# Performance work log

Measured on AMD Instinct MI355X. Metric: run time of the kernel, lower is better.

The kernel has to match this reference:

```python
import jax, jax.numpy as jnp
import numpy as np

N = 10000      # nodes
E = 160000     # edges
C = 72         # hidden dim = 18 * mul (mul=4)
A = 16         # node_attr dim (16x0e)
L = 3          # layers
O = 64         # output dim (64x0e)
B = 16         # graphs in batch
IN_DIM = 18    # irreps_node_input dim
SH = 9         # spherical harmonics dim, lmax=2
FC = 100       # radial MLP hidden (fc_neurons=[1,100])
MAX_RADIUS = 2.0
NUM_NEIGHBORS = 16.0
NUM_NODES = 625.0


def sph_harm_l2(d):
    # component-normalized real spherical harmonics up to l=2 on unit vectors d [E,3]
    x, y, z = d[:, 0], d[:, 1], d[:, 2]
    s3, s5, s15 = 3.0 ** 0.5, 5.0 ** 0.5, 15.0 ** 0.5
    return jnp.stack([
        jnp.ones_like(x),
        s3 * x, s3 * y, s3 * z,
        s15 * x * y, s15 * y * z, (s5 / 2.0) * (3.0 * z * z - 1.0),
        s15 * x * z, (s15 / 2.0) * (x * x - y * y),
    ], axis=1)  # [E, 9]


def setup_inputs() -> dict:
    key = jax.random.key(0)
    ks = jax.random.split(key, 16)
    pos = jax.random.normal(ks[0], (N, 3), dtype=jnp.float32)
    node_attr = jax.random.normal(ks[1], (N, A), dtype=jnp.float32)
    batch = jnp.sort(jax.random.randint(ks[2], (N,), 0, B))
    edge_src = jax.random.randint(ks[3], (E,), 0, N)
    edge_dst = jax.random.randint(ks[4], (E,), 0, N)
    W_in = jax.random.normal(ks[5], (IN_DIM, C), dtype=jnp.float32) / np.sqrt(IN_DIM)
    W_tp = jax.random.normal(ks[6], (L, SH, C, C), dtype=jnp.float32) / np.sqrt(C)
    W_self = jax.random.normal(ks[7], (L, C, C), dtype=jnp.float32) / np.sqrt(C)
    W_attr = jax.random.normal(ks[8], (L, A, C), dtype=jnp.float32) / np.sqrt(A)
    fc1_w = jax.random.normal(ks[9], (L, 1, FC), dtype=jnp.float32)
    fc1_b = jnp.zeros((L, FC), dtype=jnp.float32)
    fc2_w = jax.random.normal(ks[10], (L, FC, SH), dtype=jnp.float32) / np.sqrt(FC)
    W_out = jax.random.normal(ks[11], (C, O), dtype=jnp.float32) / np.sqrt(C)
    return {"pos": pos, "node_attr": node_attr, "batch": batch,
            "edge_src": edge_src, "edge_dst": edge_dst,
            "W_in": W_in, "W_tp": W_tp, "W_self": W_self, "W_attr": W_attr,
            "fc1_w": fc1_w, "fc1_b": fc1_b, "fc2_w": fc2_w, "W_out": W_out}


def reference(pos, node_attr, batch, edge_src, edge_dst,
              W_in, W_tp, W_self, W_attr, fc1_w, fc1_b, fc2_w, W_out):
    n = pos.shape[0]
    # edge geometry
    rvec = pos[edge_src] - pos[edge_dst]                      # [E,3]
    r = jnp.linalg.norm(rvec, axis=1, keepdims=True)          # [E,1]
    dvec = rvec / jnp.maximum(r, 1e-9)
    sh = sph_harm_l2(dvec)                                    # [E,9]
    # single cosine radial basis with cutoff at max_radius (number_of_basis=1)
    t = r / MAX_RADIUS
    emb = jnp.where(t < 1.0, jnp.cos(0.5 * jnp.pi * t), 0.0)  # [E,1]
    # node inputs: fixed one-hot on the scalar channel, embedded to hidden dim
    onehot = jnp.zeros((IN_DIM,), dtype=pos.dtype).at[0].set(1.0)
    h = jnp.broadcast_to((onehot @ W_in)[None, :], (n, C))    # [N,C]
    for l in range(L):
        # radial MLP -> per-edge, per-SH-path weights
        u = jax.nn.silu(emb @ fc1_w[l] + fc1_b[l]) @ fc2_w[l]  # [E,9]
        path = u * sh                                          # [E,9]
        hs = h[edge_src]                                       # [E,C]
        m = jnp.zeros_like(hs)
        for s in range(SH):  # fixed small set of tensor-product paths
            m = m + path[:, s:s + 1] * (hs @ W_tp[l, s])       # [E,C]
        agg = jax.ops.segment_sum(m, edge_dst, num_segments=n) / np.sqrt(NUM_NEIGHBORS)
        h = jax.nn.gelu(agg + h @ W_self[l] + node_attr @ W_attr[l])
    out_nodes = h @ W_out                                      # [N,O]
    pooled = jax.ops.segment_sum(out_nodes, batch, num_segments=B)
    return pooled / np.sqrt(NUM_NODES)                         # [B,O]
```

## Files before the change

kernel.cpp:

```cpp
#include <hip/hip_runtime.h>
#include <math.h>

#define NN 10000
#define NE 160000
#define CC 72
#define AA 16
#define LL 3
#define OO 64
#define NBATCH 16
#define SH 9
#define FCN 100
#define KK (SH*CC)
#define KA 736
#define KP 768
#define KG 96
#define NT 5
#define PSU 16
#define NB 1024

typedef __attribute__((ext_vector_type(8))) short bf16x8;
typedef __attribute__((ext_vector_type(4))) float f32x4;

static __device__ __forceinline__ float gelu_tanh(float x) {
    float x3 = x * x * x;
    float inner = 0.7978845608028654f * (x + 0.044715f * x3);
    return 0.5f * x * (1.0f + tanhf(inner));
}
static __device__ __forceinline__ unsigned short f2bf(float x) {
    unsigned int u = __float_as_uint(x);
    u += 0x7FFFu + ((u >> 16) & 1u);
    return (unsigned short)(u >> 16);
}
static __device__ __forceinline__ float bf2f(unsigned short u) {
    return __uint_as_float((unsigned int)u << 16);
}
static __device__ __forceinline__ unsigned int pack2bf(float lo, float hi) {
    return (unsigned int)f2bf(lo) | ((unsigned int)f2bf(hi) << 16);
}
static __device__ __forceinline__ float bfLo(unsigned int u) {
    return __uint_as_float(u << 16);
}
static __device__ __forceinline__ float bfHi(unsigned int u) {
    return __uint_as_float(u & 0xffff0000u);
}

__global__ void k_zero(int* __restrict__ cnt) {
    int i = blockIdx.x * blockDim.x + threadIdx.x;
    if (i < NN) cnt[i] = 0;
}

#define GB_HIST 625
#define GB_UTAB 13
#define GB_WCAT 180
#define GB_INIT 704
#define GB_PREP (GB_HIST + GB_UTAB + GB_WCAT + GB_INIT)

__global__ __launch_bounds__(256) void k_prep(
        const float* __restrict__ pos, const int* __restrict__ esrc,
        const int* __restrict__ edst, int* __restrict__ cnt,
        const float* __restrict__ fc1w, const float* __restrict__ fc1b,
        const float* __restrict__ fc2w, float* __restrict__ U,
        const float* __restrict__ Wtp, const float* __restrict__ Wself,
        const float* __restrict__ Wattr, unsigned short* __restrict__ Wb,
        const float* __restrict__ W_in, unsigned short* __restrict__ h0) {
    int bb = blockIdx.x, t = threadIdx.x;
    if (bb < GB_HIST) {
        int e = bb * 256 + t;
        if (e < NE) {
            int s = esrc[e], d = edst[e];
            float dx = pos[3 * s] - pos[3 * d];
            float dy = pos[3 * s + 1] - pos[3 * d + 1];
            float dz = pos[3 * s + 2] - pos[3 * d + 2];
            float r = sqrtf(dx * dx + dy * dy + dz * dz);
            if (r * 0.5f < 1.0f) atomicAdd(&cnt[d], 1);
        }
        return;
    }
    bb -= GB_HIST;
    if (bb < GB_UTAB) {
        int i = bb * 256 + t;
        if (i < LL * (NB + 1)) {
            int l = i / (NB + 1), b = i - l * (NB + 1);
            float emb = cosf(1.5707963267948966f * ((float)b / (float)NB));
            float u[SH];
#pragma unroll
            for (int q = 0; q < SH; ++q) u[q] = 0.f;
            const float* w1 = &fc1w[l * FCN];
            const float* b1 = &fc1b[l * FCN];
            const float* w2 = &fc2w[l * FCN * SH];
            for (int f = 0; f < FCN; ++f) {
                float a = emb * w1[f] + b1[f];
                float si = a / (1.0f + expf(-a));
#pragma unroll
                for (int q = 0; q < SH; ++q) u[q] += si * w2[f * SH + q];
            }
            float* ud = &U[(size_t)i * 12];
#pragma unroll
            for (int q = 0; q < SH; ++q) ud[q] = u[q];
            ud[9] = 0.f; ud[10] = 0.f; ud[11] = 0.f;
        }
        return;
    }
    bb -= GB_UTAB;
    if (bb < GB_WCAT) {
        int i0 = (bb * 256 + t) * 4;
#pragma unroll
        for (int u = 0; u < 4; ++u) {
            int i = i0 + u;
            int l = i / (NT * KG * 128);
            int rem = i - l * (NT * KG * 128);
            int nt = rem / (KG * 128); rem -= nt * (KG * 128);
            int kg = rem / 128; int e = rem - kg * 128;
            int n = nt * 16 + (e >> 3);
            int k = kg * 8 + (e & 7);
            float v = 0.f;
            if (n < CC && k < KA) {
                if (k < KK)            v = 0.25f * Wtp[(size_t)l * KK * CC + k * CC + n];
                else if (k < KK + CC)  v = Wself[(size_t)l * CC * CC + (k - KK) * CC + n];
                else                   v = Wattr[(size_t)l * AA * CC + (k - KK - CC) * CC + n];
            }
            Wb[i] = f2bf(v);
        }
        return;
    }
    bb -= GB_WCAT;
    {
        int i0 = (bb * 256 + t) * 4;
#pragma unroll
        for (int u = 0; u < 4; ++u) {
            int i = i0 + u;
            if (i < NN * CC) h0[i] = f2bf(W_in[i % CC]);
        }
    }
}

__global__ void k_scan(const int* __restrict__ cnt, int* __restrict__ off,
                       int* __restrict__ cur, float* __restrict__ hp) {
    __shared__ int sa[256], sb[256];
    const int PER = 40;
    int t = threadIdx.x;
    int base = t * PER;
    int loc[PER];
    int run = 0;
#pragma unroll
    for (int i = 0; i < PER; ++i) {
        int idx = base + i;
        int v = (idx < NN) ? cnt[idx] : 0;
        loc[i] = run;
        run += v;
    }
    sa[t] = run;
    __syncthreads();
    int* in = sa; int* out = sb;
    for (int o = 1; o < 256; o <<= 1) {
        int v = in[t];
        if (t >= o) v += in[t - o];
        out[t] = v;
        __syncthreads();
        int* tmp = in; in = out; out = tmp;
    }
    int ebase = (t > 0) ? in[t - 1] : 0;
#pragma unroll
    for (int i = 0; i < PER; ++i) {
        int idx = base + i;
        if (idx <= NN) {
            int v = ebase + loc[i];
            off[idx] = v;
            if (idx < NN) cur[idx] = v;
        }
    }
    for (int i = t; i < NBATCH * CC; i += 256) hp[i] = 0.f;
}

__global__ __launch_bounds__(256) void k_scatter3(const float* __restrict__ pos,
                                                  const int* __restrict__ esrc,
                                                  const int* __restrict__ edst,
                                                  int* __restrict__ cur,
                                                  int* __restrict__ src_s,
                                                  const float* __restrict__ U,
                                                  unsigned short* __restrict__ path) {
    int e = blockIdx.x * blockDim.x + threadIdx.x;
    if (e >= NE) return;
    int s = esrc[e], d = edst[e];
    float dx = pos[3 * s] - pos[3 * d];
    float dy = pos[3 * s + 1] - pos[3 * d + 1];
    float dz = pos[3 * s + 2] - pos[3 * d + 2];
    float r = sqrtf(dx * dx + dy * dy + dz * dz);
    if (r * 0.5f >= 1.0f) return;
    int slot = atomicAdd(&cur[d], 1);
    src_s[slot] = s;

    float inv = 1.0f / fmaxf(r, 1e-9f);
    float x = dx * inv, y = dy * inv, z = dz * inv;
    const float s3 = 1.7320508075688772f;
    const float s5 = 2.23606797749979f;
    const float s15 = 3.872983346207417f;
    float sh[SH];
    sh[0] = 1.0f;
    sh[1] = s3 * x;
    sh[2] = s3 * y;
    sh[3] = s3 * z;
    sh[4] = s15 * x * y;
    sh[5] = s15 * y * z;
    sh[6] = 0.5f * s5 * (3.0f * z * z - 1.0f);
    sh[7] = s15 * x * z;
    sh[8] = 0.5f * s15 * (x * x - y * y);

    float fb = r * 0.5f * (float)NB;
    int b0 = (int)fb;
    float fr = fb - (float)b0;

#pragma unroll
    for (int l = 0; l < LL; ++l) {
        const float* t0 = &U[((size_t)l * (NB + 1) + b0) * 12];
        float4 a0 = *(const float4*)(t0 + 0);
        float4 a1 = *(const float4*)(t0 + 4);
        float  a2 = t0[8];
        float4 c0 = *(const float4*)(t0 + 12);
        float4 c1 = *(const float4*)(t0 + 16);
        float  c2 = t0[20];
        float u0 = (a0.x + fr * (c0.x - a0.x)) * sh[0];
        float u1 = (a0.y + fr * (c0.y - a0.y)) * sh[1];
        float u2 = (a0.z + fr * (c0.z - a0.z)) * sh[2];
        float u3 = (a0.w + fr * (c0.w - a0.w)) * sh[3];
        float u4 = (a1.x + fr * (c1.x - a1.x)) * sh[4];
        float u5 = (a1.y + fr * (c1.y - a1.y)) * sh[5];
        float u6 = (a1.z + fr * (c1.z - a1.z)) * sh[6];
        float u7 = (a1.w + fr * (c1.w - a1.w)) * sh[7];
        float u8 = (a2   + fr * (c2   - a2))   * sh[8];
        unsigned short* pd = &path[((size_t)l * NE + slot) * PSU];
        uint4 w0, w1;
        w0.x = pack2bf(u0, u1); w0.y = pack2bf(u2, u3);
        w0.z = pack2bf(u4, u5); w0.w = pack2bf(u6, u7);
        w1.x = pack2bf(u8, 0.f); w1.y = 0u; w1.z = 0u; w1.w = 0u;
        *(uint4*)pd = w0;
        *(uint4*)(pd + 8) = w1;
    }
}

__global__ __launch_bounds__(1024, 8) void k_layer(
        const unsigned short* __restrict__ h,
        const float* __restrict__ attr,
        const unsigned short* __restrict__ path_l,
        const int* __restrict__ src_s,
        const int* __restrict__ off,
        const unsigned short* __restrict__ Wb,
        unsigned short* __restrict__ hout) {
    __shared__ unsigned short Alds[KG * 128];
    int t = threadIdx.x, w = t >> 6, lane = t & 63;
    int n0 = blockIdx.x * 16;
    int d = n0 + w;
    int db = off[d], de = off[d + 1];

    bool act = lane < 36;
    int c2 = 2 * lane;
    float a1[SH], a2[SH];
#pragma unroll
    for (int q = 0; q < SH; ++q) { a1[q] = 0.f; a2[q] = 0.f; }

    for (int i = db; i < de; i += 4) {
        int m = de - i;
        unsigned int hv[4];
        uint4 pa[4];
        unsigned int pb[4];
#pragma unroll
        for (int j = 0; j < 4; ++j) {
            if (j < m) {
                int s = src_s[i + j];
                pa[j] = *(const uint4*)&path_l[(size_t)(i + j) * PSU];
                pb[j] = *(const unsigned int*)&path_l[(size_t)(i + j) * PSU + 8];
                if (act) hv[j] = *(const unsigned int*)&h[(size_t)s * CC + c2];
            }
        }
#pragma unroll
        for (int j = 0; j < 4; ++j) {
            if (j < m) {
                float lo = act ? bfLo(hv[j]) : 0.f;
                float hi = act ? bfHi(hv[j]) : 0.f;
                float p0 = bfLo(pa[j].x), p1 = bfHi(pa[j].x);
                float p2 = bfLo(pa[j].y), p3 = bfHi(pa[j].y);
                float p4 = bfLo(pa[j].z), p5 = bfHi(pa[j].z);
                float p6 = bfLo(pa[j].w), p7 = bfHi(pa[j].w);
                float p8 = bfLo(pb[j]);
                a1[0] += p0 * lo; a2[0] += p0 * hi;
                a1[1] += p1 * lo; a2[1] += p1 * hi;
                a1[2] += p2 * lo; a2[2] += p2 * hi;
                a1[3] += p3 * lo; a2[3] += p3 * hi;
                a1[4] += p4 * lo; a2[4] += p4 * hi;
                a1[5] += p5 * lo; a2[5] += p5 * hi;
                a1[6] += p6 * lo; a2[6] += p6 * hi;
                a1[7] += p7 * lo; a2[7] += p7 * hi;
                a1[8] += p8 * lo; a2[8] += p8 * hi;
            }
        }
    }

    if (act) {
        int kgo = lane >> 2, kjo = 2 * (lane & 3);
        int hb = w * 8 + kjo;
#pragma unroll
        for (int q = 0; q < SH; ++q)
            *(unsigned int*)&Alds[(9 * q + kgo) * 128 + hb] = pack2bf(a1[q], a2[q]);
        *(unsigned int*)&Alds[(81 + kgo) * 128 + hb] =
            *(const unsigned int*)&h[(size_t)d * CC + c2];
        if (lane < 8)
            *(unsigned int*)&Alds[(90 + kgo) * 128 + hb] =
                pack2bf(attr[(size_t)d * AA + c2], attr[(size_t)d * AA + c2 + 1]);
    }
    if (lane < 16)
        *(unsigned int*)&Alds[(92 + (lane >> 2)) * 128 + w * 8 + 2 * (lane & 3)] = 0u;
    __syncthreads();

    if (w < NT) {
        const unsigned short* Ab = Alds + (lane & 15) * 8;
        const unsigned short* Bb = Wb + ((size_t)w * KG) * 128 + (lane & 15) * 8;
        f32x4 acc = (f32x4){0.f, 0.f, 0.f, 0.f};
#pragma unroll
        for (int s = 0; s < 24; ++s) {
            int kg = s * 4 + (lane >> 4);
            bf16x8 af = *(const bf16x8*)(Ab + (size_t)kg * 128);
            bf16x8 bq = *(const bf16x8*)(Bb + (size_t)kg * 128);
            acc = __builtin_amdgcn_mfma_f32_16x16x32_bf16(af, bq, acc, 0, 0, 0);
        }
        int cb = lane & 15, rb = (lane >> 4) * 4;
        int row = n0 + rb, col = w * 16 + cb;
        if (col < CC) {
#pragma unroll
            for (int j = 0; j < 4; ++j)
                hout[(size_t)(row + j) * CC + col] = f2bf(gelu_tanh(acc[j]));
        }
    }
}

__global__ __launch_bounds__(256) void k_pool(const unsigned short* __restrict__ h,
                                              const int* __restrict__ batch,
                                              float* __restrict__ hp) {
    __shared__ float sp[NBATCH * CC];
    int t = threadIdx.x;
    for (int i = t; i < NBATCH * CC; i += 256) sp[i] = 0.f;
    __syncthreads();
    int n0 = blockIdx.x * 16;
    for (int i = t; i < 16 * CC; i += 256) {
        int nl = i / CC, c = i - nl * CC;
        int n = n0 + nl;
        if (n < NN) atomicAdd(&sp[batch[n] * CC + c], bf2f(h[(size_t)n * CC + c]));
    }
    __syncthreads();
    for (int i = t; i < NBATCH * CC; i += 256) {
        float v = sp[i];
        if (v != 0.f) atomicAdd(&hp[i], v);
    }
}

__global__ __launch_bounds__(1024) void k_outmm(const float* __restrict__ hp,
                                                const float* __restrict__ Wout,
                                                float* __restrict__ out) {
    __shared__ float hs[NBATCH * CC];
    int t = threadIdx.x;
    for (int i = t; i < NBATCH * CC; i += 1024) hs[i] = hp[i];
    __syncthreads();
    int b = t >> 6, o = t & 63;
    float acc = 0.f;
#pragma unroll 8
    for (int c = 0; c < CC; ++c) acc += hs[b * CC + c] * Wout[c * OO + o];
    out[t] = acc * (1.0f / 25.0f);
}

extern "C" void kernel_launch(void* const* d_in, const int* in_sizes, int n_in,
                              void* d_out, int out_size, void* d_ws, size_t ws_size,
                              hipStream_t stream) {
    const float* pos       = (const float*)d_in[0];
    const float* node_attr = (const float*)d_in[1];
    const int*   batch     = (const int*)d_in[2];
    const int*   esrc      = (const int*)d_in[3];
    const int*   edst      = (const int*)d_in[4];
    const float* W_in      = (const float*)d_in[5];
    const float* W_tp      = (const float*)d_in[6];
    const float* W_self    = (const float*)d_in[7];
    const float* W_attr    = (const float*)d_in[8];
    const float* fc1w      = (const float*)d_in[9];
    const float* fc1b      = (const float*)d_in[10];
    const float* fc2w      = (const float*)d_in[11];
    const float* W_out     = (const float*)d_in[12];
    float* out = (float*)d_out;

    char* p = (char*)d_ws;
    auto alloc = [&](size_t bytes) -> void* {
        void* r = (void*)p;
        p += (bytes + 255) & ~(size_t)255;
        return r;
    };
    int*   cnt   = (int*)alloc((size_t)NN * 4);
    int*   cur   = (int*)alloc((size_t)NN * 4);
    float* hp    = (float*)alloc((size_t)NBATCH * CC * 4);
    int*   off   = (int*)alloc((size_t)(NN + 1) * 4);
    int*   src_s = (int*)alloc((size_t)NE * 4);
    unsigned short* path = (unsigned short*)alloc((size_t)LL * NE * PSU * 2);
    float* U     = (float*)alloc((size_t)LL * (NB + 1) * 12 * 4);
    unsigned short* Wb = (unsigned short*)alloc((size_t)LL * NT * KG * 128 * 2);
    unsigned short* h0 = (unsigned short*)alloc((size_t)NN * CC * 2);
    unsigned short* h1 = (unsigned short*)alloc((size_t)NN * CC * 2);

    k_zero<<<(NN + 255) / 256, 256, 0, stream>>>(cnt);
    k_prep<<<GB_PREP, 256, 0, stream>>>(pos, esrc, edst, cnt, fc1w, fc1b, fc2w, U,
                                        W_tp, W_self, W_attr, Wb, W_in, h0);
    k_scan<<<1, 256, 0, stream>>>(cnt, off, cur, hp);
    k_scatter3<<<(NE + 255) / 256, 256, 0, stream>>>(pos, esrc, edst, cur, src_s, U, path);

    const unsigned short* hin = h0;
    unsigned short* hout = h1;
    for (int l = 0; l < LL; ++l) {
        k_layer<<<NN / 16, 1024, 0, stream>>>(hin, node_attr,
                                              path + (size_t)l * NE * PSU, src_s, off,
                                              Wb + (size_t)l * NT * KG * 128, hout);
        const unsigned short* tmp = hin; hin = hout; hout = (unsigned short*)tmp;
    }
    k_pool<<<(NN + 15) / 16, 256, 0, stream>>>(hin, batch, hp);
    k_outmm<<<1, 1024, 0, stream>>>(hp, W_out, out);
}
```

Before: 161.2 us.

## Stage block's per-edge path weights in LDS and deepen gather unroll to 8

Each block now copies the contiguous path-weight rows for all edges of its 16 destination nodes into shared memory in chunks, using cooperative vector loads. Each wave then reads the path weights from LDS instead of issuing redundant per-lane global loads. The gather of source features is unrolled to 8 edges for more memory-level parallelism. In exchange it adds block-wide barriers per chunk, extra LDS usage, and possible load imbalance across waves within a chunk.

```diff
diff --git a/kernel.cpp b/kernel.cpp
--- a/kernel.cpp
+++ b/kernel.cpp
@@ -17,6 +17,7 @@
 #define NT 5
 #define PSU 16
 #define NB 1024
+#define EMAX 176
 
 typedef __attribute__((ext_vector_type(8))) short bf16x8;
 typedef __attribute__((ext_vector_type(4))) float f32x4;
@@ -246,10 +247,12 @@
         const int* __restrict__ off,
         const unsigned short* __restrict__ Wb,
         unsigned short* __restrict__ hout) {
+    __shared__ unsigned short Plds[EMAX * PSU];
     __shared__ unsigned short Alds[KG * 128];
     int t = threadIdx.x, w = t >> 6, lane = t & 63;
     int n0 = blockIdx.x * 16;
     int d = n0 + w;
+    int b0 = off[n0], e0 = off[n0 + 16];
     int db = off[d], de = off[d + 1];
 
     bool act = lane < 36;
@@ -258,41 +261,51 @@
 #pragma unroll
     for (int q = 0; q < SH; ++q) { a1[q] = 0.f; a2[q] = 0.f; }
 
-    for (int i = db; i < de; i += 4) {
-        int m = de - i;
-        unsigned int hv[4];
-        uint4 pa[4];
-        unsigned int pb[4];
-#pragma unroll
-        for (int j = 0; j < 4; ++j) {
-            if (j < m) {
-                int s = src_s[i + j];
-                pa[j] = *(const uint4*)&path_l[(size_t)(i + j) * PSU];
-                pb[j] = *(const unsigned int*)&path_l[(size_t)(i + j) * PSU + 8];
-                if (act) hv[j] = *(const unsigned int*)&h[(size_t)s * CC + c2];
+    for (int base = b0; base < e0; base += EMAX) {
+        int nE = min(EMAX, e0 - base);
+        const uint4* p4 = (const uint4*)(path_l + (size_t)base * PSU);
+        uint4* Pl4 = (uint4*)Plds;
+        for (int idx = t; idx < nE * 2; idx += 1024)
+            Pl4[idx] = p4[idx];
+        __syncthreads();
+        int lb = db > base ? db : base;
+        int le = de < base + nE ? de : base + nE;
+        for (int i = lb; i < le; i += 8) {
+            int m = le - i;
+            unsigned int hv[8];
+#pragma unroll
+            for (int j = 0; j < 8; ++j) {
+                if (j < m && act) {
+                    int s = src_s[i + j];
+                    hv[j] = *(const unsigned int*)&h[(size_t)s * CC + c2];
+                }
             }
-        }
-#pragma unroll
-        for (int j = 0; j < 4; ++j) {
-            if (j < m) {
-                float lo = act ? bfLo(hv[j]) : 0.f;
-                float hi = act ? bfHi(hv[j]) : 0.f;
-                float p0 = bfLo(pa[j].x), p1 = bfHi(pa[j].x);
-                float p2 = bfLo(pa[j].y), p3 = bfHi(pa[j].y);
-                float p4 = bfLo(pa[j].z), p5 = bfHi(pa[j].z);
-                float p6 = bfLo(pa[j].w), p7 = bfHi(pa[j].w);
-                float p8 = bfLo(pb[j]);
-                a1[0] += p0 * lo; a2[0] += p0 * hi;
-                a1[1] += p1 * lo; a2[1] += p1 * hi;
-                a1[2] += p2 * lo; a2[2] += p2 * hi;
-                a1[3] += p3 * lo; a2[3] += p3 * hi;
-                a1[4] += p4 * lo; a2[4] += p4 * hi;
-                a1[5] += p5 * lo; a2[5] += p5 * hi;
-                a1[6] += p6 * lo; a2[6] += p6 * hi;
-                a1[7] += p7 * lo; a2[7] += p7 * hi;
-                a1[8] += p8 * lo; a2[8] += p8 * hi;
+#pragma unroll
+            for (int j = 0; j < 8; ++j) {
+                if (j < m) {
+                    const unsigned short* p = &Plds[(i + j - base) * PSU];
+                    uint4 pw = *(const uint4*)p;
+                    unsigned int pz = *(const unsigned int*)(p + 8);
+                    float lo = act ? bfLo(hv[j]) : 0.f;
+                    float hi = act ? bfHi(hv[j]) : 0.f;
+                    float p0 = bfLo(pw.x), p1 = bfHi(pw.x);
+                    float p2 = bfLo(pw.y), p3 = bfHi(pw.y);
+                    float p4v = bfLo(pw.z), p5 = bfHi(pw.z);
+                    float p6 = bfLo(pw.w), p7 = bfHi(pw.w);
+                    float p8 = bfLo(pz);
+                    a1[0] += p0 * lo;  a2[0] += p0 * hi;
+                    a1[1] += p1 * lo;  a2[1] += p1 * hi;
+                    a1[2] += p2 * lo;  a2[2] += p2 * hi;
+                    a1[3] += p3 * lo;  a2[3] += p3 * hi;
+                    a1[4] += p4v * lo; a2[4] += p4v * hi;
+                    a1[5] += p5 * lo;  a2[5] += p5 * hi;
+                    a1[6] += p6 * lo;  a2[6] += p6 * hi;
+                    a1[7] += p7 * lo;  a2[7] += p7 * hi;
+                    a1[8] += p8 * lo;  a2[8] += p8 * hi;
+                }
             }
         }
+        __syncthreads();
     }
 
     if (act) {
```

Result: faster. 138.5 us (-14.1%).

## Store compact per-edge geometry and recompute path weights inside layer kernel

Applied to the files above, without the earlier changes.

The scatter kernel now writes one 16-byte record per edge (source index, bf16 direction, radial bin position) instead of a source index array plus three layers of 32-byte bf16 path-weight rows. Each layer kernel rebuilds the spherical harmonics and interpolates the radial lookup table itself. This shrinks scatter writes and per-layer edge reads, at the cost of extra ALU work and table loads in the layer loop. The unit-direction components are now rounded to bf16, which changes precision slightly.

```diff
diff --git a/kernel.cpp b/kernel.cpp
--- a/kernel.cpp
+++ b/kernel.cpp
@@ -12,10 +12,8 @@
 #define FCN 100
 #define KK (SH*CC)
 #define KA 736
-#define KP 768
 #define KG 96
 #define NT 5
-#define PSU 16
 #define NB 1024
 
 typedef __attribute__((ext_vector_type(8))) short bf16x8;
@@ -172,13 +170,11 @@
     for (int i = t; i < NBATCH * CC; i += 256) hp[i] = 0.f;
 }
 
-__global__ __launch_bounds__(256) void k_scatter3(const float* __restrict__ pos,
+__global__ __launch_bounds__(256) void k_scatter4(const float* __restrict__ pos,
                                                   const int* __restrict__ esrc,
                                                   const int* __restrict__ edst,
                                                   int* __restrict__ cur,
-                                                  int* __restrict__ src_s,
-                                                  const float* __restrict__ U,
-                                                  unsigned short* __restrict__ path) {
+                                                  uint4* __restrict__ geom) {
     int e = blockIdx.x * blockDim.x + threadIdx.x;
     if (e >= NE) return;
     int s = esrc[e], d = edst[e];
@@ -188,62 +184,23 @@
     float r = sqrtf(dx * dx + dy * dy + dz * dz);
     if (r * 0.5f >= 1.0f) return;
     int slot = atomicAdd(&cur[d], 1);
-    src_s[slot] = s;
-
     float inv = 1.0f / fmaxf(r, 1e-9f);
     float x = dx * inv, y = dy * inv, z = dz * inv;
-    const float s3 = 1.7320508075688772f;
-    const float s5 = 2.23606797749979f;
-    const float s15 = 3.872983346207417f;
-    float sh[SH];
-    sh[0] = 1.0f;
-    sh[1] = s3 * x;
-    sh[2] = s3 * y;
-    sh[3] = s3 * z;
-    sh[4] = s15 * x * y;
-    sh[5] = s15 * y * z;
-    sh[6] = 0.5f * s5 * (3.0f * z * z - 1.0f);
-    sh[7] = s15 * x * z;
-    sh[8] = 0.5f * s15 * (x * x - y * y);
-
     float fb = r * 0.5f * (float)NB;
-    int b0 = (int)fb;
-    float fr = fb - (float)b0;
-
-#pragma unroll
-    for (int l = 0; l < LL; ++l) {
-        const float* t0 = &U[((size_t)l * (NB + 1) + b0) * 12];
-        float4 a0 = *(const float4*)(t0 + 0);
-        float4 a1 = *(const float4*)(t0 + 4);
-        float  a2 = t0[8];
-        float4 c0 = *(const float4*)(t0 + 12);
-        float4 c1 = *(const float4*)(t0 + 16);
-        float  c2 = t0[20];
-        float u0 = (a0.x + fr * (c0.x - a0.x)) * sh[0];
-        float u1 = (a0.y + fr * (c0.y - a0.y)) * sh[1];
-        float u2 = (a0.z + fr * (c0.z - a0.z)) * sh[2];
-        float u3 = (a0.w + fr * (c0.w - a0.w)) * sh[3];
-        float u4 = (a1.x + fr * (c1.x - a1.x)) * sh[4];
-        float u5 = (a1.y + fr * (c1.y - a1.y)) * sh[5];
-        float u6 = (a1.z + fr * (c1.z - a1.z)) * sh[6];
-        float u7 = (a1.w + fr * (c1.w - a1.w)) * sh[7];
-        float u8 = (a2   + fr * (c2   - a2))   * sh[8];
-        unsigned short* pd = &path[((size_t)l * NE + slot) * PSU];
-        uint4 w0, w1;
-        w0.x = pack2bf(u0, u1); w0.y = pack2bf(u2, u3);
-        w0.z = pack2bf(u4, u5); w0.w = pack2bf(u6, u7);
-        w1.x = pack2bf(u8, 0.f); w1.y = 0u; w1.z = 0u; w1.w = 0u;
-        *(uint4*)pd = w0;
-        *(uint4*)(pd + 8) = w1;
-    }
+    uint4 g;
+    g.x = (unsigned int)s;
+    g.y = pack2bf(x, y);
+    g.z = pack2bf(z, 0.f);
+    g.w = __float_as_uint(fb);
+    geom[slot] = g;
 }
 
 __global__ __launch_bounds__(1024, 8) void k_layer(
         const unsigned short* __restrict__ h,
         const float* __restrict__ attr,
-        const unsigned short* __restrict__ path_l,
-        const int* __restrict__ src_s,
+        const uint4* __restrict__ geom,
         const int* __restrict__ off,
+        const float* __restrict__ Ul,
         const unsigned short* __restrict__ Wb,
         unsigned short* __restrict__ hout) {
     __shared__ unsigned short Alds[KG * 128];
@@ -252,6 +209,10 @@
     int d = n0 + w;
     int db = off[d], de = off[d + 1];
 
+    const float s3 = 1.7320508075688772f;
+    const float s5 = 2.23606797749979f;
+    const float s15 = 3.872983346207417f;
+
     bool act = lane < 36;
     int c2 = 2 * lane;
     float a1[SH], a2[SH];
@@ -260,28 +221,40 @@
 
     for (int i = db; i < de; i += 4) {
         int m = de - i;
+        uint4 g[4];
         unsigned int hv[4];
-        uint4 pa[4];
-        unsigned int pb[4];
+#pragma unroll
+        for (int j = 0; j < 4; ++j)
+            if (j < m) g[j] = geom[i + j];
+#pragma unroll
+        for (int j = 0; j < 4; ++j)
+            if (j < m && act)
+                hv[j] = *(const unsigned int*)&h[(size_t)g[j].x * CC + c2];
 #pragma unroll
         for (int j = 0; j < 4; ++j) {
             if (j < m) {
-                int s = src_s[i + j];
-                pa[j] = *(const uint4*)&path_l[(size_t)(i + j) * PSU];
-                pb[j] = *(const unsigned int*)&path_l[(size_t)(i + j) * PSU + 8];
-                if (act) hv[j] = *(const unsigned int*)&h[(size_t)s * CC + c2];
-            }
-        }
-#pragma unroll
-        for (int j = 0; j < 4; ++j) {
-            if (j < m) {
+                float x = bfLo(g[j].y), y = bfHi(g[j].y), z = bfLo(g[j].z);
+                float fb = __uint_as_float(g[j].w);
+                int b0 = (int)fb;
+                float fr = fb - (float)b0;
+                const float* t0 = &Ul[(size_t)b0 * 12];
+                float4 ua = *(const float4*)(t0 + 0);
+                float4 ub = *(const float4*)(t0 + 4);
+                float  uc = t0[8];
+                float4 va = *(const float4*)(t0 + 12);
+                float4 vb = *(const float4*)(t0 + 16);
+                float  vc = t0[20];
+                float p0 = (ua.x + fr * (va.x - ua.x));
+                float p1 = (ua.y + fr * (va.y - ua.y)) * (s3 * x);
+                float p2 = (ua.z + fr * (va.z - ua.z)) * (s3 * y);
+                float p3 = (ua.w + fr * (va.w - ua.w)) * (s3 * z);
+                float p4 = (ub.x + fr * (vb.x - ub.x)) * (s15 * x * y);
+                float p5 = (ub.y + fr * (vb.y - ub.y)) * (s15 * y * z);
+                float p6 = (ub.z + fr * (vb.z - ub.z)) * (0.5f * s5 * (3.0f * z * z - 1.0f));
+                float p7 = (ub.w + fr * (vb.w - ub.w)) * (s15 * x * z);
+                float p8 = (uc   + fr * (vc   - uc))   * (0.5f * s15 * (x * x - y * y));
                 float lo = act ? bfLo(hv[j]) : 0.f;
                 float hi = act ? bfHi(hv[j]) : 0.f;
-                float p0 = bfLo(pa[j].x), p1 = bfHi(pa[j].x);
-                float p2 = bfLo(pa[j].y), p3 = bfHi(pa[j].y);
-                float p4 = bfLo(pa[j].z), p5 = bfHi(pa[j].z);
-                float p6 = bfLo(pa[j].w), p7 = bfHi(pa[j].w);
-                float p8 = bfLo(pb[j]);
                 a1[0] += p0 * lo; a2[0] += p0 * hi;
                 a1[1] += p1 * lo; a2[1] += p1 * hi;
                 a1[2] += p2 * lo; a2[2] += p2 * hi;
@@ -394,8 +367,7 @@
     int*   cur   = (int*)alloc((size_t)NN * 4);
     float* hp    = (float*)alloc((size_t)NBATCH * CC * 4);
     int*   off   = (int*)alloc((size_t)(NN + 1) * 4);
-    int*   src_s = (int*)alloc((size_t)NE * 4);
-    unsigned short* path = (unsigned short*)alloc((size_t)LL * NE * PSU * 2);
+    uint4* geom  = (uint4*)alloc((size_t)NE * 16);
     float* U     = (float*)alloc((size_t)LL * (NB + 1) * 12 * 4);
     unsigned short* Wb = (unsigned short*)alloc((size_t)LL * NT * KG * 128 * 2);
     unsigned short* h0 = (unsigned short*)alloc((size_t)NN * CC * 2);
@@ -405,13 +377,13 @@
     k_prep<<<GB_PREP, 256, 0, stream>>>(pos, esrc, edst, cnt, fc1w, fc1b, fc2w, U,
                                         W_tp, W_self, W_attr, Wb, W_in, h0);
     k_scan<<<1, 256, 0, stream>>>(cnt, off, cur, hp);
-    k_scatter3<<<(NE + 255) / 256, 256, 0, stream>>>(pos, esrc, edst, cur, src_s, U, path);
+    k_scatter4<<<(NE + 255) / 256, 256, 0, stream>>>(pos, esrc, edst, cur, geom);
 
     const unsigned short* hin = h0;
     unsigned short* hout = h1;
     for (int l = 0; l < LL; ++l) {
-        k_layer<<<NN / 16, 1024, 0, stream>>>(hin, node_attr,
-                                              path + (size_t)l * NE * PSU, src_s, off,
+        k_layer<<<NN / 16, 1024, 0, stream>>>(hin, node_attr, geom, off,
+                                              U + (size_t)l * (NB + 1) * 12,
                                               Wb + (size_t)l * NT * KG * 128, hout);
         const unsigned short* tmp = hin; hin = hout; hout = (unsigned short*)tmp;
     }
```

Result: slower. 388.9 us (+141.3%).
